# Optimization experiments

Hardware: AMD Instinct MI355X
Metric: run time of the kernel (lower is better)

## Reference

```python
import jax, jax.numpy as jnp
import numpy as np

N_HEAD = 16  # from init_kwargs

def setup_inputs() -> dict:
    key = jax.random.key(0)
    k1, k2, k3 = jax.random.split(key, 3)
    B, T, C = 2, 2048, 1024
    x = jax.random.normal(k1, (B, T, C), dtype=jnp.float32)
    W_qkv = jax.random.normal(k2, (3 * C, C), dtype=jnp.float32) * (1.0 / np.sqrt(C))
    W_proj = jax.random.normal(k3, (C, C), dtype=jnp.float32) * (1.0 / np.sqrt(C))
    b_proj = jnp.zeros((C,), dtype=jnp.float32)
    return {"x": x, "W_qkv": W_qkv, "W_proj": W_proj, "b_proj": b_proj}

def reference(x, W_qkv, W_proj, b_proj):
    B, T, C = x.shape
    H = N_HEAD
    hs = C // H
    # QKV projection (bias=False), split heads
    qkv = (x @ W_qkv.T).reshape(B, T, 3, H, hs)
    q = jnp.transpose(qkv[:, :, 0], (0, 2, 1, 3))  # [B,H,T,hs]
    k = jnp.transpose(qkv[:, :, 1], (0, 2, 1, 3))
    v = jnp.transpose(qkv[:, :, 2], (0, 2, 1, 3))
    scale = np.float32(1.0 / np.sqrt(hs))
    s = jnp.einsum('bhqd,bhkd->bhqk', q, k) * scale  # [B,H,T,T]
    # sp2norm: softplus weights, causal-masked, normalized by row L2 norm
    w = jax.nn.softplus(s)
    causal = jnp.tril(jnp.ones((T, T), dtype=bool))
    w = jnp.where(causal[None, None], w, jnp.float32(0.0))
    norm = jnp.sqrt(jnp.sum(w * w, axis=-1, keepdims=True))  # [B,H,T,1]
    out = jnp.einsum('bhqk,bhkd->bhqd', w, v) / norm  # [B,H,T,hs]
    out = jnp.transpose(out, (0, 2, 1, 3)).reshape(B, T, C)
    return out @ W_proj.T + b_proj
```

## Files before the change

kernel.cpp:

```cpp
#include <hip/hip_runtime.h>
#include <cstdint>
#include <cstddef>

typedef __bf16 bf16_t;
typedef __bf16 bf16x8 __attribute__((ext_vector_type(8)));
typedef __bf16 bf16x4 __attribute__((ext_vector_type(4)));
typedef float  f32x4  __attribute__((ext_vector_type(4)));

#define MFMA_BF16(a, b, c) __builtin_amdgcn_mfma_f32_16x16x32_bf16((a), (b), (c), 0, 0, 0)

__device__ __forceinline__ void async_load16(const void* g, void* l) {
    __builtin_amdgcn_global_load_lds((const __attribute__((address_space(1))) void*)g,
                                     (__attribute__((address_space(3))) void*)l,
                                     16, 0, 0);
}

#define SWZ(r, cg) ((((r) << 3) | ((cg) ^ ((r) & 7))) << 3)

#define Bq   2
#define Tq   2048
#define Cq   1024
#define Hq   16
#define HSq  64
#define Mrows 4096

__global__ __launch_bounds__(256)
void cvt_all(const float* __restrict__ x, const float* __restrict__ wqkv,
             const float* __restrict__ wproj,
             bf16_t* __restrict__ xb, bf16_t* __restrict__ wqkvb,
             bf16_t* __restrict__ wprojb) {
    size_t gid = (size_t)blockIdx.x * 256 + threadIdx.x;
    const float* src; bf16_t* dst; size_t off;
    if (gid < 1048576)      { src = x;     dst = xb;     off = gid; }
    else if (gid < 1835008) { src = wqkv;  dst = wqkvb;  off = gid - 1048576; }
    else                    { src = wproj; dst = wprojb; off = gid - 1835008; }
    float4 v = ((const float4*)src)[off];
    bf16x4 o;
    o[0] = (bf16_t)v.x; o[1] = (bf16_t)v.y; o[2] = (bf16_t)v.z; o[3] = (bf16_t)v.w;
    *(bf16x4*)(dst + off * 4) = o;
}

template <int BM, int EPI>
__global__ __launch_bounds__(256)
void gemm_bt(const bf16_t* __restrict__ A, const bf16_t* __restrict__ B,
             void* __restrict__ Cout, const float* __restrict__ bias,
             bf16_t* __restrict__ qc, bf16_t* __restrict__ kc, bf16_t* __restrict__ vtp,
             int M, int N, int K) {
    constexpr int MR = BM / 32;
    constexpr int ACH = BM * 8 / 256;
    __shared__ __align__(16) bf16_t As[BM * 64];
    __shared__ __align__(16) bf16_t Bs[128 * 64];

    const int tid  = threadIdx.x;
    const int wave = tid >> 6;
    const int lane = tid & 63;
    const int m0 = blockIdx.y * BM;
    const int n0 = blockIdx.x * 128;
    const int wm = (wave >> 1) * (BM / 2);
    const int wn = (wave & 1) * 64;
    const int lrow = lane & 15;
    const int lg   = lane >> 4;

    f32x4 acc[MR][4] = {};

    const bf16_t* Ag = A + (size_t)m0 * K;
    const bf16_t* Bg = B + (size_t)n0 * K;

    for (int k0 = 0; k0 < K; k0 += 64) {
        #pragma unroll
        for (int i = 0; i < ACH; i++) {
            int s = i * 256 + tid;
            int r = s >> 3, cg = (s & 7) ^ (r & 7);
            async_load16(Ag + (size_t)r * K + k0 + cg * 8, &As[s * 8]);
        }
        #pragma unroll
        for (int i = 0; i < 4; i++) {
            int s = i * 256 + tid;
            int r = s >> 3, cg = (s & 7) ^ (r & 7);
            async_load16(Bg + (size_t)r * K + k0 + cg * 8, &Bs[s * 8]);
        }
        __syncthreads();

        #pragma unroll
        for (int kk = 0; kk < 2; kk++) {
            bf16x8 af[MR], bfr[4];
            #pragma unroll
            for (int r = 0; r < MR; r++)
                af[r] = *(const bf16x8*)&As[SWZ(wm + r * 16 + lrow, kk * 4 + lg)];
            #pragma unroll
            for (int c = 0; c < 4; c++)
                bfr[c] = *(const bf16x8*)&Bs[SWZ(wn + c * 16 + lrow, kk * 4 + lg)];
            #pragma unroll
            for (int r = 0; r < MR; r++)
                #pragma unroll
                for (int c = 0; c < 4; c++)
                    acc[r][c] = MFMA_BF16(af[r], bfr[c], acc[r][c]);
        }
        __syncthreads();
    }

    const int er = (lane >> 4) * 4;
    const int ec = lane & 15;
    #pragma unroll
    for (int r = 0; r < MR; r++) {
        #pragma unroll
        for (int c = 0; c < 4; c++) {
            int m = m0 + wm + r * 16 + er;
            int n = n0 + wn + c * 16 + ec;
            if (EPI == 1) {
                #pragma unroll
                for (int v = 0; v < 4; v++)
                    ((float*)Cout)[(size_t)(m + v) * N + n] = acc[r][c][v] + bias[n];
            } else {
                int bb = m >> 11, t = m & 2047;
                if (n < 1024) {
                    #pragma unroll
                    for (int v = 0; v < 4; v++)
                        qc[(size_t)(m + v) * 1024 + n] = (bf16_t)acc[r][c][v];
                } else if (n < 2048) {
                    int h = (n - 1024) >> 6, d = (n - 1024) & 63;
                    bf16_t* p = kc + ((size_t)(bb * 16 + h) * Tq + t) * 64 + d;
                    #pragma unroll
                    for (int v = 0; v < 4; v++) p[v * 64] = (bf16_t)acc[r][c][v];
                } else {
                    int h = (n - 2048) >> 6, d = (n - 2048) & 63;
                    bf16x4 o;
                    #pragma unroll
                    for (int v = 0; v < 4; v++) o[v] = (bf16_t)acc[r][c][v];
                    *(bf16x4*)&vtp[((size_t)(bb * 16 + h) * 64 + d) * Tq + t] = o;
                }
            }
        }
    }
}

__global__ __launch_bounds__(256)
void attn_kernel(const bf16_t* __restrict__ Qc, const bf16_t* __restrict__ Kc,
                 const bf16_t* __restrict__ Vt,
                 bf16_t* __restrict__ Op0, bf16_t* __restrict__ Op1,
                 bf16_t* __restrict__ Op2, bf16_t* __restrict__ Op3,
                 float* __restrict__ n2part) {
    __shared__ __align__(16) bf16_t Ks[64 * 64];
    __shared__ __align__(16) bf16_t Vs[64 * 64];
    __shared__ __align__(16) bf16_t Ws[64 * 64];

    const int tid = threadIdx.x;
    const int wave = tid >> 6;
    const int lane = tid & 63;
    const int lrow = lane & 15;
    const int lg   = lane >> 4;
    const int er = lg * 4;
    const int ec = lane & 15;

    const int raw     = blockIdx.x;
    const int qi      = 31 - (raw >> 2);
    const int quarter = raw & 3;
    const int q0      = qi * 64;
    const int bh = blockIdx.y;
    const int b = bh >> 4, h = bh & 15;

    const int nt = qi + 1;
    const int lo = (quarter * nt) >> 2;
    const int hi = ((quarter + 1) * nt) >> 2;

    const bf16_t* Qb = Qc + (size_t)b * Tq * Cq + h * 64;
    const bf16_t* Kb = Kc + (size_t)bh * Tq * 64;
    const bf16_t* Vb = Vt + (size_t)bh * 64 * Tq;

    bf16x8 qf[2];
    {
        const bf16_t* qrow = Qb + (size_t)(q0 + wave * 16 + lrow) * Cq + lg * 8;
        qf[0] = *(const bf16x8*)(qrow);
        qf[1] = *(const bf16x8*)(qrow + 32);
    }

    const int s0 = tid, s1 = tid + 256;
    const int r0 = s0 >> 3, cg0 = (s0 & 7) ^ (r0 & 7);
    const int r1 = s1 >> 3, cg1 = (s1 & 7) ^ (r1 & 7);

    bf16x8 kr0, kr1, vr0, vr1;
    if (lo < hi) {
        const int key0 = lo * 64;
        kr0 = *(const bf16x8*)&Kb[(size_t)(key0 + r0) * 64 + cg0 * 8];
        kr1 = *(const bf16x8*)&Kb[(size_t)(key0 + r1) * 64 + cg1 * 8];
        vr0 = *(const bf16x8*)&Vb[(size_t)r0 * Tq + key0 + cg0 * 8];
        vr1 = *(const bf16x8*)&Vb[(size_t)r1 * Tq + key0 + cg1 * 8];
    }

    f32x4 oacc[4] = {};
    float n2 = 0.f;
    const float C1 = 0.18033688f;

    for (int kt = lo; kt < hi; kt++) {
        __syncthreads();
        *(bf16x8*)&Ks[s0 * 8] = kr0;
        *(bf16x8*)&Ks[s1 * 8] = kr1;
        *(bf16x8*)&Vs[s0 * 8] = vr0;
        *(bf16x8*)&Vs[s1 * 8] = vr1;
        __syncthreads();

        if (kt + 1 < hi) {
            const int k1 = (kt + 1) * 64;
            kr0 = *(const bf16x8*)&Kb[(size_t)(k1 + r0) * 64 + cg0 * 8];
            kr1 = *(const bf16x8*)&Kb[(size_t)(k1 + r1) * 64 + cg1 * 8];
            vr0 = *(const bf16x8*)&Vb[(size_t)r0 * Tq + k1 + cg0 * 8];
            vr1 = *(const bf16x8*)&Vb[(size_t)r1 * Tq + k1 + cg1 * 8];
        }

        f32x4 sacc[4];
        #pragma unroll
        for (int j = 0; j < 4; j++) {
            int r = j * 16 + lrow;
            bf16x8 kf0 = *(const bf16x8*)&Ks[SWZ(r, lg)];
            bf16x8 kf1 = *(const bf16x8*)&Ks[SWZ(r, 4 + lg)];
            f32x4 z = {};
            z = MFMA_BF16(kf0, qf[0], z);
            sacc[j] = MFMA_BF16(kf1, qf[1], z);
        }

        const bool diag = (kt == qi);
        #pragma unroll
        for (int j = 0; j < 4; j++) {
            bf16x4 wb;
            #pragma unroll
            for (int v = 0; v < 4; v++) {
                float t = sacc[j][v] * C1;
                float e = __builtin_amdgcn_exp2f(-fabsf(t));
                float w = fmaxf(t, 0.f) + __builtin_amdgcn_logf(1.f + e);
                if (diag && (j * 16 + er + v > wave * 16 + ec)) w = 0.f;
                n2 += w * w;
                wb[v] = (bf16_t)w;
            }
            *(bf16x4*)&Ws[SWZ(wave * 16 + ec, 2 * j + (lg >> 1)) + (lg & 1) * 4] = wb;
        }

        #pragma unroll
        for (int s2 = 0; s2 < 2; s2++) {
            bf16x8 wf = *(const bf16x8*)&Ws[SWZ(wave * 16 + lrow, s2 * 4 + lg)];
            #pragma unroll
            for (int jd = 0; jd < 4; jd++) {
                bf16x8 vf = *(const bf16x8*)&Vs[SWZ(jd * 16 + lrow, s2 * 4 + lg)];
                oacc[jd] = MFMA_BF16(wf, vf, oacc[jd]);
            }
        }
    }

    n2 += __shfl_xor(n2, 16, 64);
    n2 += __shfl_xor(n2, 32, 64);

    bf16_t* Op = (quarter == 0 ? Op0 : quarter == 1 ? Op1 : quarter == 2 ? Op2 : Op3)
               + ((size_t)bh * 32 + qi) * 4096;
    #pragma unroll
    for (int jd = 0; jd < 4; jd++) {
        #pragma unroll
        for (int v = 0; v < 4; v++) {
            Op[(wave * 16 + er + v) * 64 + jd * 16 + ec] = (bf16_t)oacc[jd][v];
        }
    }
    if (lg == 0) {
        n2part[((size_t)quarter * 1024 + bh * 32 + qi) * 64 + wave * 16 + ec] = n2;
    }
}

__global__ __launch_bounds__(256)
void combine_kernel(const bf16_t* __restrict__ O0, const bf16_t* __restrict__ O1,
                    const bf16_t* __restrict__ O2, const bf16_t* __restrict__ O3,
                    const float* __restrict__ n2part, bf16_t* __restrict__ ao) {
    const int qi = blockIdx.x;
    const int bh = blockIdx.y;
    const int b = bh >> 4, h = bh & 15;
    const int t = threadIdx.x;
    const size_t base = ((size_t)bh * 32 + qi) * 4096;
    const float* np = n2part + ((size_t)bh * 32 + qi) * 64;
    #pragma unroll
    for (int i = 0; i < 2; i++) {
        int idx = i * 2048 + t * 8;
        int row = idx >> 6, col = idx & 63;
        bf16x8 a0 = *(const bf16x8*)(O0 + base + idx);
        bf16x8 a1 = *(const bf16x8*)(O1 + base + idx);
        bf16x8 a2 = *(const bf16x8*)(O2 + base + idx);
        bf16x8 a3 = *(const bf16x8*)(O3 + base + idx);
        float nsum = np[row] + np[(size_t)1024 * 64 + row]
                   + np[(size_t)2048 * 64 + row] + np[(size_t)3072 * 64 + row];
        float inv = rsqrtf(nsum);
        bf16x8 o;
        #pragma unroll
        for (int j = 0; j < 8; j++)
            o[j] = (bf16_t)(((float)a0[j] + (float)a1[j] + (float)a2[j] + (float)a3[j]) * inv);
        *(bf16x8*)(ao + (size_t)(b * Tq + qi * 64 + row) * Cq + h * HSq + col) = o;
    }
}

extern "C" void kernel_launch(void* const* d_in, const int* in_sizes, int n_in,
                              void* d_out, int out_size, void* d_ws, size_t ws_size,
                              hipStream_t stream) {
    const float* x     = (const float*)d_in[0];
    const float* wqkv  = (const float*)d_in[1];
    const float* wproj = (const float*)d_in[2];
    const float* bproj = (const float*)d_in[3];
    float* out = (float*)d_out;

    char* ws = (char*)d_ws;
    bf16_t* wprojb = (bf16_t*)(ws);
    bf16_t* xb     = (bf16_t*)(ws + ( 2u << 20));
    bf16_t* wqkvb  = (bf16_t*)(ws + (10u << 20));
    bf16_t* qcb    = (bf16_t*)(ws + (16u << 20));
    bf16_t* kcb    = (bf16_t*)(ws + (24u << 20));
    bf16_t* vtb    = (bf16_t*)(ws + (32u << 20));
    bf16_t* opart0 = (bf16_t*)(ws + ( 2u << 20));
    float*  n2part = (float*)(ws + (10u << 20));
    bf16_t* opart1 = (bf16_t*)(ws + (40u << 20));
    bf16_t* opart2 = (bf16_t*)(ws + (48u << 20));
    bf16_t* opart3 = (bf16_t*)(ws + (56u << 20));
    bf16_t* aob    = (bf16_t*)(ws + (24u << 20));

    cvt_all<<<8192, 256, 0, stream>>>(x, wqkv, wproj, xb, wqkvb, wprojb);

    gemm_bt<128, 2><<<dim3(24, 32), 256, 0, stream>>>(xb, wqkvb, nullptr, nullptr,
                                                      qcb, kcb, vtb, Mrows, 3 * Cq, Cq);
    attn_kernel<<<dim3(128, 32), 256, 0, stream>>>(qcb, kcb, vtb,
                                                   opart0, opart1, opart2, opart3, n2part);
    combine_kernel<<<dim3(32, 32), 256, 0, stream>>>(opart0, opart1, opart2, opart3,
                                                     n2part, aob);
    gemm_bt<64, 1><<<dim3(8, 64), 256, 0, stream>>>(aob, wprojb, (void*)out, bproj,
                                                    nullptr, nullptr, nullptr, Mrows, Cq, Cq);
}
```

Measured before the change: 188.0 us.

## Split attention KV range in halves and fuse combine into output projection GEMM

The attention kernel now splits each query tile's key range into two parts instead of four, halving the partial outputs and norm partials. The separate combine kernel is removed. Its work (summing the partials, applying the rsqrt of the summed norms, converting to bf16) now happens inside the output-projection GEMM's A-tile load, so the intermediate attention output never round-trips through global memory. The costs are fewer attention blocks to fill the device, and synchronous, recomputed partial loads in the GEMM prologue, which repeat across the 8 N-blocks.

```diff
diff --git a/kernel.cpp b/kernel.cpp
--- a/kernel.cpp
+++ b/kernel.cpp
@@ -40,58 +40,49 @@
     *(bf16x4*)(dst + off * 4) = o;
 }
 
-template <int BM, int EPI>
 __global__ __launch_bounds__(256)
-void gemm_bt(const bf16_t* __restrict__ A, const bf16_t* __restrict__ B,
-             void* __restrict__ Cout, const float* __restrict__ bias,
-             bf16_t* __restrict__ qc, bf16_t* __restrict__ kc, bf16_t* __restrict__ vtp,
-             int M, int N, int K) {
-    constexpr int MR = BM / 32;
-    constexpr int ACH = BM * 8 / 256;
-    __shared__ __align__(16) bf16_t As[BM * 64];
+void gemm_qkv(const bf16_t* __restrict__ A, const bf16_t* __restrict__ B,
+              bf16_t* __restrict__ qc, bf16_t* __restrict__ kc, bf16_t* __restrict__ vtp,
+              int M, int N, int K) {
+    __shared__ __align__(16) bf16_t As[128 * 64];
     __shared__ __align__(16) bf16_t Bs[128 * 64];
 
     const int tid  = threadIdx.x;
     const int wave = tid >> 6;
     const int lane = tid & 63;
-    const int m0 = blockIdx.y * BM;
+    const int m0 = blockIdx.y * 128;
     const int n0 = blockIdx.x * 128;
-    const int wm = (wave >> 1) * (BM / 2);
+    const int wm = (wave >> 1) * 64;
     const int wn = (wave & 1) * 64;
     const int lrow = lane & 15;
     const int lg   = lane >> 4;
 
-    f32x4 acc[MR][4] = {};
+    f32x4 acc[4][4] = {};
 
     const bf16_t* Ag = A + (size_t)m0 * K;
     const bf16_t* Bg = B + (size_t)n0 * K;
 
     for (int k0 = 0; k0 < K; k0 += 64) {
         #pragma unroll
-        for (int i = 0; i < ACH; i++) {
+        for (int i = 0; i < 4; i++) {
             int s = i * 256 + tid;
             int r = s >> 3, cg = (s & 7) ^ (r & 7);
             async_load16(Ag + (size_t)r * K + k0 + cg * 8, &As[s * 8]);
-        }
-        #pragma unroll
-        for (int i = 0; i < 4; i++) {
-            int s = i * 256 + tid;
-            int r = s >> 3, cg = (s & 7) ^ (r & 7);
             async_load16(Bg + (size_t)r * K + k0 + cg * 8, &Bs[s * 8]);
         }
         __syncthreads();
 
         #pragma unroll
         for (int kk = 0; kk < 2; kk++) {
-            bf16x8 af[MR], bfr[4];
-            #pragma unroll
-            for (int r = 0; r < MR; r++)
+            bf16x8 af[4], bfr[4];
+            #pragma unroll
+            for (int r = 0; r < 4; r++)
                 af[r] = *(const bf16x8*)&As[SWZ(wm + r * 16 + lrow, kk * 4 + lg)];
             #pragma unroll
             for (int c = 0; c < 4; c++)
                 bfr[c] = *(const bf16x8*)&Bs[SWZ(wn + c * 16 + lrow, kk * 4 + lg)];
             #pragma unroll
-            for (int r = 0; r < MR; r++)
+            for (int r = 0; r < 4; r++)
                 #pragma unroll
                 for (int c = 0; c < 4; c++)
                     acc[r][c] = MFMA_BF16(af[r], bfr[c], acc[r][c]);
@@ -102,33 +93,27 @@
     const int er = (lane >> 4) * 4;
     const int ec = lane & 15;
     #pragma unroll
-    for (int r = 0; r < MR; r++) {
+    for (int r = 0; r < 4; r++) {
         #pragma unroll
         for (int c = 0; c < 4; c++) {
             int m = m0 + wm + r * 16 + er;
             int n = n0 + wn + c * 16 + ec;
-            if (EPI == 1) {
+            int bb = m >> 11, t = m & 2047;
+            if (n < 1024) {
                 #pragma unroll
                 for (int v = 0; v < 4; v++)
-                    ((float*)Cout)[(size_t)(m + v) * N + n] = acc[r][c][v] + bias[n];
+                    qc[(size_t)(m + v) * 1024 + n] = (bf16_t)acc[r][c][v];
+            } else if (n < 2048) {
+                int h = (n - 1024) >> 6, d = (n - 1024) & 63;
+                bf16_t* p = kc + ((size_t)(bb * 16 + h) * Tq + t) * 64 + d;
+                #pragma unroll
+                for (int v = 0; v < 4; v++) p[v * 64] = (bf16_t)acc[r][c][v];
             } else {
-                int bb = m >> 11, t = m & 2047;
-                if (n < 1024) {
-                    #pragma unroll
-                    for (int v = 0; v < 4; v++)
-                        qc[(size_t)(m + v) * 1024 + n] = (bf16_t)acc[r][c][v];
-                } else if (n < 2048) {
-                    int h = (n - 1024) >> 6, d = (n - 1024) & 63;
-                    bf16_t* p = kc + ((size_t)(bb * 16 + h) * Tq + t) * 64 + d;
-                    #pragma unroll
-                    for (int v = 0; v < 4; v++) p[v * 64] = (bf16_t)acc[r][c][v];
-                } else {
-                    int h = (n - 2048) >> 6, d = (n - 2048) & 63;
-                    bf16x4 o;
-                    #pragma unroll
-                    for (int v = 0; v < 4; v++) o[v] = (bf16_t)acc[r][c][v];
-                    *(bf16x4*)&vtp[((size_t)(bb * 16 + h) * 64 + d) * Tq + t] = o;
-                }
+                int h = (n - 2048) >> 6, d = (n - 2048) & 63;
+                bf16x4 o;
+                #pragma unroll
+                for (int v = 0; v < 4; v++) o[v] = (bf16_t)acc[r][c][v];
+                *(bf16x4*)&vtp[((size_t)(bb * 16 + h) * 64 + d) * Tq + t] = o;
             }
         }
     }
@@ -138,7 +123,6 @@
 void attn_kernel(const bf16_t* __restrict__ Qc, const bf16_t* __restrict__ Kc,
                  const bf16_t* __restrict__ Vt,
                  bf16_t* __restrict__ Op0, bf16_t* __restrict__ Op1,
-                 bf16_t* __restrict__ Op2, bf16_t* __restrict__ Op3,
                  float* __restrict__ n2part) {
     __shared__ __align__(16) bf16_t Ks[64 * 64];
     __shared__ __align__(16) bf16_t Vs[64 * 64];
@@ -152,16 +136,17 @@
     const int er = lg * 4;
     const int ec = lane & 15;
 
-    const int raw     = blockIdx.x;
-    const int qi      = 31 - (raw >> 2);
-    const int quarter = raw & 3;
-    const int q0      = qi * 64;
+    const int raw  = blockIdx.x;
+    const int qi   = 31 - (raw >> 1);
+    const int half = raw & 1;
+    const int q0   = qi * 64;
     const int bh = blockIdx.y;
     const int b = bh >> 4, h = bh & 15;
 
     const int nt = qi + 1;
-    const int lo = (quarter * nt) >> 2;
-    const int hi = ((quarter + 1) * nt) >> 2;
+    const int nh = (nt + 1) >> 1;
+    const int lo = half ? nh : 0;
+    const int hi = half ? nt : nh;
 
     const bf16_t* Qb = Qc + (size_t)b * Tq * Cq + h * 64;
     const bf16_t* Kb = Kc + (size_t)bh * Tq * 64;
@@ -248,8 +233,7 @@
     n2 += __shfl_xor(n2, 16, 64);
     n2 += __shfl_xor(n2, 32, 64);
 
-    bf16_t* Op = (quarter == 0 ? Op0 : quarter == 1 ? Op1 : quarter == 2 ? Op2 : Op3)
-               + ((size_t)bh * 32 + qi) * 4096;
+    bf16_t* Op = (half ? Op1 : Op0) + ((size_t)bh * 32 + qi) * 4096;
     #pragma unroll
     for (int jd = 0; jd < 4; jd++) {
         #pragma unroll
@@ -258,36 +242,101 @@
         }
     }
     if (lg == 0) {
-        n2part[((size_t)quarter * 1024 + bh * 32 + qi) * 64 + wave * 16 + ec] = n2;
+        n2part[((size_t)half * 1024 + bh * 32 + qi) * 64 + wave * 16 + ec] = n2;
     }
 }
 
 __global__ __launch_bounds__(256)
-void combine_kernel(const bf16_t* __restrict__ O0, const bf16_t* __restrict__ O1,
-                    const bf16_t* __restrict__ O2, const bf16_t* __restrict__ O3,
-                    const float* __restrict__ n2part, bf16_t* __restrict__ ao) {
-    const int qi = blockIdx.x;
-    const int bh = blockIdx.y;
-    const int b = bh >> 4, h = bh & 15;
-    const int t = threadIdx.x;
-    const size_t base = ((size_t)bh * 32 + qi) * 4096;
-    const float* np = n2part + ((size_t)bh * 32 + qi) * 64;
+void gemm_out(const bf16_t* __restrict__ O0, const bf16_t* __restrict__ O1,
+              const float* __restrict__ n2part, const bf16_t* __restrict__ B,
+              float* __restrict__ Cout, const float* __restrict__ bias,
+              int M, int N, int K) {
+    __shared__ __align__(16) bf16_t As[64 * 64];
+    __shared__ __align__(16) bf16_t Bs[128 * 64];
+
+    const int tid  = threadIdx.x;
+    const int wave = tid >> 6;
+    const int lane = tid & 63;
+    const int m0 = blockIdx.y * 64;
+    const int n0 = blockIdx.x * 128;
+    const int wm = (wave >> 1) * 32;
+    const int wn = (wave & 1) * 64;
+    const int lrow = lane & 15;
+    const int lg   = lane >> 4;
+
+    const int bb = m0 >> 11;
+    const int qi = (m0 >> 6) & 31;
+
+    f32x4 acc[2][4] = {};
+
+    const bf16_t* Bg = B + (size_t)n0 * K;
+
+    const int sA0 = tid, sA1 = tid + 256;
+    const int rA0 = sA0 >> 3, cgA0 = (sA0 & 7) ^ (rA0 & 7);
+    const int rA1 = sA1 >> 3, cgA1 = (sA1 & 7) ^ (rA1 & 7);
+
+    for (int k0 = 0; k0 < K; k0 += 64) {
+        const int h = k0 >> 6;
+        const size_t tb = ((size_t)(bb * 16 + h) * 32 + qi) * 4096;
+        const float* np = n2part + ((size_t)(bb * 16 + h) * 32 + qi) * 64;
+        {
+            size_t pa = tb + rA0 * 64 + cgA0 * 8;
+            bf16x8 a0 = *(const bf16x8*)&O0[pa];
+            bf16x8 a1 = *(const bf16x8*)&O1[pa];
+            float inv = rsqrtf(np[rA0] + np[(size_t)1024 * 64 + rA0]);
+            bf16x8 o;
+            #pragma unroll
+            for (int j = 0; j < 8; j++) o[j] = (bf16_t)(((float)a0[j] + (float)a1[j]) * inv);
+            *(bf16x8*)&As[sA0 * 8] = o;
+        }
+        {
+            size_t pa = tb + rA1 * 64 + cgA1 * 8;
+            bf16x8 a0 = *(const bf16x8*)&O0[pa];
+            bf16x8 a1 = *(const bf16x8*)&O1[pa];
+            float inv = rsqrtf(np[rA1] + np[(size_t)1024 * 64 + rA1]);
+            bf16x8 o;
+            #pragma unroll
+            for (int j = 0; j < 8; j++) o[j] = (bf16_t)(((float)a0[j] + (float)a1[j]) * inv);
+            *(bf16x8*)&As[sA1 * 8] = o;
+        }
+        #pragma unroll
+        for (int i = 0; i < 4; i++) {
+            int s = i * 256 + tid;
+            int r = s >> 3, cg = (s & 7) ^ (r & 7);
+            async_load16(Bg + (size_t)r * K + k0 + cg * 8, &Bs[s * 8]);
+        }
+        __syncthreads();
+
+        #pragma unroll
+        for (int kk = 0; kk < 2; kk++) {
+            bf16x8 af[2], bfr[4];
+            #pragma unroll
+            for (int r = 0; r < 2; r++)
+                af[r] = *(const bf16x8*)&As[SWZ(wm + r * 16 + lrow, kk * 4 + lg)];
+            #pragma unroll
+            for (int c = 0; c < 4; c++)
+                bfr[c] = *(const bf16x8*)&Bs[SWZ(wn + c * 16 + lrow, kk * 4 + lg)];
+            #pragma unroll
+            for (int r = 0; r < 2; r++)
+                #pragma unroll
+                for (int c = 0; c < 4; c++)
+                    acc[r][c] = MFMA_BF16(af[r], bfr[c], acc[r][c]);
+        }
+        __syncthreads();
+    }
+
+    const int er = (lane >> 4) * 4;
+    const int ec = lane & 15;
     #pragma unroll
-    for (int i = 0; i < 2; i++) {
-        int idx = i * 2048 + t * 8;
-        int row = idx >> 6, col = idx & 63;
-        bf16x8 a0 = *(const bf16x8*)(O0 + base + idx);
-        bf16x8 a1 = *(const bf16x8*)(O1 + base + idx);
-        bf16x8 a2 = *(const bf16x8*)(O2 + base + idx);
-        bf16x8 a3 = *(const bf16x8*)(O3 + base + idx);
-        float nsum = np[row] + np[(size_t)1024 * 64 + row]
-                   + np[(size_t)2048 * 64 + row] + np[(size_t)3072 * 64 + row];
-        float inv = rsqrtf(nsum);
-        bf16x8 o;
-        #pragma unroll
-        for (int j = 0; j < 8; j++)
-            o[j] = (bf16_t)(((float)a0[j] + (float)a1[j] + (float)a2[j] + (float)a3[j]) * inv);
-        *(bf16x8*)(ao + (size_t)(b * Tq + qi * 64 + row) * Cq + h * HSq + col) = o;
+    for (int r = 0; r < 2; r++) {
+        #pragma unroll
+        for (int c = 0; c < 4; c++) {
+            int m = m0 + wm + r * 16 + er;
+            int n = n0 + wn + c * 16 + ec;
+            #pragma unroll
+            for (int v = 0; v < 4; v++)
+                Cout[(size_t)(m + v) * N + n] = acc[r][c][v] + bias[n];
+        }
     }
 }
 
@@ -310,18 +359,12 @@
     bf16_t* opart0 = (bf16_t*)(ws + ( 2u << 20));
     float*  n2part = (float*)(ws + (10u << 20));
     bf16_t* opart1 = (bf16_t*)(ws + (40u << 20));
-    bf16_t* opart2 = (bf16_t*)(ws + (48u << 20));
-    bf16_t* opart3 = (bf16_t*)(ws + (56u << 20));
-    bf16_t* aob    = (bf16_t*)(ws + (24u << 20));
 
     cvt_all<<<8192, 256, 0, stream>>>(x, wqkv, wproj, xb, wqkvb, wprojb);
 
-    gemm_bt<128, 2><<<dim3(24, 32), 256, 0, stream>>>(xb, wqkvb, nullptr, nullptr,
-                                                      qcb, kcb, vtb, Mrows, 3 * Cq, Cq);
-    attn_kernel<<<dim3(128, 32), 256, 0, stream>>>(qcb, kcb, vtb,
-                                                   opart0, opart1, opart2, opart3, n2part);
-    combine_kernel<<<dim3(32, 32), 256, 0, stream>>>(opart0, opart1, opart2, opart3,
-                                                     n2part, aob);
-    gemm_bt<64, 1><<<dim3(8, 64), 256, 0, stream>>>(aob, wprojb, (void*)out, bproj,
-                                                    nullptr, nullptr, nullptr, Mrows, Cq, Cq);
-}
+    gemm_qkv<<<dim3(24, 32), 256, 0, stream>>>(xb, wqkvb, qcb, kcb, vtb,
+                                               Mrows, 3 * Cq, Cq);
+    attn_kernel<<<dim3(64, 32), 256, 0, stream>>>(qcb, kcb, vtb, opart0, opart1, n2part);
+    gemm_out<<<dim3(8, 64), 256, 0, stream>>>(opart0, opart1, n2part, wprojb,
+                                              out, bproj, Mrows, Cq, Cq);
+}
```

After: 196.2 us. 1.04x slower.
